# Kernel tuning notes

Hardware: AMD Instinct MI355X
Metric: run time of the kernel (lower is better)

## Reference

```python
import jax, jax.numpy as jnp
from jax import lax
import numpy as np

B, H, W = 8, 512, 512
HW = H * W  # sentinel label for non-mask pixels


def _label_components(mask):
    """4-connectivity connected-component labeling (min flat-index per component).
    mask: [H,W] bool. Returns [HW] int32 labels; non-mask pixels get label HW.
    Label propagation + pointer jumping -> O(log diameter) iterations."""
    idx = jnp.arange(HW, dtype=jnp.int32).reshape(H, W)
    lab0 = jnp.where(mask, idx, HW)

    def step(lab):
        p = jnp.pad(lab, 1, mode='constant', constant_values=HW)
        nb = jnp.minimum(jnp.minimum(p[:-2, 1:-1], p[2:, 1:-1]),
                         jnp.minimum(p[1:-1, :-2], p[1:-1, 2:]))
        new = jnp.where(mask, jnp.minimum(lab, nb), HW)
        flat = new.reshape(-1)
        flat_ext = jnp.concatenate([flat, jnp.array([HW], dtype=flat.dtype)])
        new = jnp.minimum(flat, flat_ext[flat]).reshape(H, W)  # pointer jump
        return jnp.where(mask, new, HW)

    def cond(state):
        return state[1]

    def body(state):
        lab, _ = state
        new = step(lab)
        return new, jnp.any(new != lab)

    lab, _ = lax.while_loop(cond, body, (lab0, jnp.array(True)))
    return lab.reshape(-1)


def _keep_large(mask):
    """Keep pixels belonging to components with area > max_area/2 (matches
    ndi.label + ndi.sum + thresholded relabel; ndi.sum scaling by 255/1 cancels)."""
    labels = _label_components(mask)  # [HW]
    counts = jax.ops.segment_sum(mask.reshape(-1).astype(jnp.float32), labels,
                                 num_segments=HW + 1)  # counts[HW]=0 (non-mask contributes 0)
    max_area = counts.max()
    keep = mask.reshape(-1) & (counts[labels] > 0.5 * max_area)
    return keep.reshape(mask.shape)


def _masked_ce(logits, target):
    """CrossEntropyLoss(ignore_index=255, reduction='mean'). logits [B,C,H,W], target [B,H,W]."""
    logp = jax.nn.log_softmax(logits, axis=1)
    valid = target != 255
    tc = jnp.where(valid, target, 0)
    nll = -jnp.take_along_axis(logp, tc[:, None], axis=1)[:, 0]  # [B,H,W]
    denom = jnp.maximum(jnp.sum(valid), 1).astype(logp.dtype)
    return jnp.sum(jnp.where(valid, nll, 0.0)) / denom


def setup_inputs() -> dict:
    key = jax.random.key(0)
    k1, k2 = jax.random.split(key)
    preds = jax.random.normal(k1, (3, B, 2, H, W), dtype=jnp.float32)
    cams = jax.random.uniform(k2, (B, 1, H, W), dtype=jnp.float32)
    return {"preds": preds, "cams": cams}


def reference(preds, cams):
    cam = cams[:, 0]                      # [B,H,W]
    bg_mask = cam >= 0.2                  # pixels left at 255 in bg_label (the labeled regions)
    fg_mask = cam > 0.6                   # pixels set to 1 in fg_label
    keep_bg = jax.vmap(_keep_large)(bg_mask)
    keep_fg = jax.vmap(_keep_large)(fg_mask)
    bg_t = jnp.where(keep_bg, 255, 0).astype(jnp.int32)   # large uncertain regions ignored
    fg_t = jnp.where(keep_fg, 1, 255).astype(jnp.int32)   # small/non-fg ignored
    loss = jnp.float32(0.0)
    for i in range(preds.shape[0]):       # weight (1**i / 1) == 1
        loss = loss + _masked_ce(preds[i], fg_t) + _masked_ce(preds[i], bg_t)
    return loss
```

## Files before the change

### kernel.cpp

```cpp
#include <hip/hip_runtime.h>
#include <hip/hip_bf16.h>
#include <math.h>

#define Bsz    8
#define Wdim   512
#define HWv    (512 * 512)
#define LOG2HW 18
#define NIMG   16
#define TILE   64
#define TPIX   (TILE * TILE)
#define CEBLK  6144
#define CNTBLK 2048


__device__ __forceinline__ int uf_find(int* L, int x) {
  int p = L[x];
  while (p != x) {
    int gp = L[p];
    if (gp != p) atomicMin(&L[x], gp);
    x = gp;
    p = L[x];
  }
  return x;
}

__device__ __forceinline__ int find_ro(const int* __restrict__ L, int x) {
  int p = L[x];
  while (p != x) { x = p; p = L[x]; }
  return x;
}

__device__ __forceinline__ void uf_union(int* L, int a, int b) {
  a = uf_find(L, a);
  b = uf_find(L, b);
  while (a != b) {
    if (a < b) { int t = a; a = b; b = t; }
    int old = atomicMin(&L[a], b);
    if (old == a) return;
    a = old;
  }
}


__global__ __launch_bounds__(1024) void k_local(const float* __restrict__ cams,
                                                int* __restrict__ labels,
                                                int* __restrict__ areas) {
  int img  = blockIdx.x >> 6;
  int tile = blockIdx.x & 63;
  int tY = tile >> 3, tX = tile & 7;
  int b = img & 7;
  bool fg = (img & 8) != 0;
  int gbase = img << LOG2HW;
  int oy = tY * TILE, ox = tX * TILE;
  int lane = threadIdx.x & 63;

  __shared__ int P[TPIX];
  __shared__ int A[TPIX];

  #pragma unroll
  for (int it = 0; it < 4; ++it) {
    int i  = it * 1024 + threadIdx.x;
    int ly = i >> 6;
    float c = cams[(b << LOG2HW) + ((oy + ly) << 9) + (ox + lane)];
    bool m = fg ? (c > 0.6f) : (c >= 0.2f);
    unsigned long long bm = __ballot(m);
    int par = -1;
    if (m) {
      unsigned long long below = (1ULL << lane) - 1ULL;
      unsigned long long z = (~bm) & below;
      int rs = z ? (64 - __clzll(z)) : 0;
      par = (ly << 6) + rs;
    }
    P[i] = par;
    A[i] = 0;
  }
  __syncthreads();

  #pragma unroll
  for (int it = 0; it < 4; ++it) {
    int i = it * 1024 + threadIdx.x;
    if (i >= TILE && P[i] >= 0 && P[i - TILE] >= 0) {
      bool skip = (lane > 0) && (P[i - 1] >= 0) && (P[i - TILE - 1] >= 0);
      if (!skip) uf_union(P, i, i - TILE);
    }
  }
  __syncthreads();

  #pragma unroll
  for (int it = 0; it < 4; ++it) {
    int i = it * 1024 + threadIdx.x;
    bool m = P[i] >= 0;
    unsigned long long bm = __ballot(m);
    int rs = 0;
    if (m) {
      unsigned long long below = (1ULL << lane) - 1ULL;
      unsigned long long z = (~bm) & below;
      rs = z ? (64 - __clzll(z)) : 0;
    }
    bool isStart = m && (rs == lane);
    int r = -1;
    if (isStart) r = find_ro(P, i);
    int root = __shfl(r, rs);
    if (m) P[i] = root;
    if (isStart) {
      unsigned long long t = (~bm) >> lane;
      int runlen = t ? (__ffsll((long long)t) - 1) : (64 - lane);
      atomicAdd(&A[root], runlen);
    }
  }
  __syncthreads();

  #pragma unroll
  for (int it = 0; it < 4; ++it) {
    int i  = it * 1024 + threadIdx.x;
    int ly = i >> 6;
    int g  = ((oy + ly) << 9) + (ox + lane);
    int p  = P[i];
    int lab = -1;
    if (p >= 0) lab = ((oy + (p >> 6)) << 9) + (ox + (p & 63));
    labels[gbase + g] = lab;
    areas[gbase + g]  = (p == i) ? A[i] : 0;
  }
}

__global__ void k_border(int* __restrict__ labels, int* __restrict__ maxa) {
  if (blockIdx.x == 0) {
    if (threadIdx.x < NIMG) maxa[threadIdx.x] = 0;
  }
  const int per_img = 14 * Wdim;
  int t = blockIdx.x * blockDim.x + threadIdx.x;
  if (t >= NIMG * per_img) return;
  int img = t / per_img;
  int r   = t - img * per_img;
  int k = r >> 9, j = r & (Wdim - 1);
  int* L = labels + (img << LOG2HW);
  if (k < 7) {
    int x = TILE * k + (TILE - 1);
    int p = (j << 9) + x, q = p + 1;
    if (L[p] >= 0 && L[q] >= 0) {
      bool skip = (j > 0) && (L[p - Wdim] >= 0) && (L[q - Wdim] >= 0);
      if (!skip) uf_union(L, p, q);
    }
  } else {
    int y = TILE * (k - 7) + (TILE - 1);
    int p = (y << 9) + j, q = p + Wdim;
    if (L[p] >= 0 && L[q] >= 0) {
      bool skip = (j > 0) && (L[p - 1] >= 0) && (L[q - 1] >= 0);
      if (!skip) uf_union(L, p, q);
    }
  }
}

__global__ void k_flatten(int* __restrict__ labels, int* __restrict__ areas) {
  int t = blockIdx.x * blockDim.x + threadIdx.x;
  int idx0 = t << 2;
  int4 ar = *(const int4*)&areas[idx0];
  if ((ar.x | ar.y | ar.z | ar.w) <= 0) return;
  int img  = idx0 >> LOG2HW;
  int base = img << LOG2HW;
  int* L = labels + base;
  int self0 = idx0 - base;
  int4 lab = *(const int4*)&labels[idx0];
  if (ar.x > 0) { int r = find_ro(L, lab.x); L[self0]     = r; if (r != self0)     atomicAdd(&areas[base + r], ar.x); }
  if (ar.y > 0) { int r = find_ro(L, lab.y); L[self0 + 1] = r; if (r != self0 + 1) atomicAdd(&areas[base + r], ar.y); }
  if (ar.z > 0) { int r = find_ro(L, lab.z); L[self0 + 2] = r; if (r != self0 + 2) atomicAdd(&areas[base + r], ar.z); }
  if (ar.w > 0) { int r = find_ro(L, lab.w); L[self0 + 3] = r; if (r != self0 + 3) atomicAdd(&areas[base + r], ar.w); }
}

__global__ void k_max(const int* __restrict__ areas, int* __restrict__ maxa) {
  int img = blockIdx.x >> 4;
  int seg = blockIdx.x & 15;
  const int4* a4 = (const int4*)(areas + (img << LOG2HW));
  int base = seg * (HWv / 4 / 16);
  int m = 0;
  #pragma unroll
  for (int k = 0; k < 16; ++k) {
    int4 v = a4[base + k * 256 + threadIdx.x];
    m = max(m, max(max(v.x, v.y), max(v.z, v.w)));
  }
  #pragma unroll
  for (int off = 32; off > 0; off >>= 1)
    m = max(m, __shfl_down(m, off));
  __shared__ int lm[4];
  int wave = threadIdx.x >> 6;
  if ((threadIdx.x & 63) == 0) lm[wave] = m;
  __syncthreads();
  if (threadIdx.x == 0) {
    int bm = max(max(lm[0], lm[1]), max(lm[2], lm[3]));
    if (bm > 0) atomicMax(&maxa[img], bm);
  }
}

__global__ __launch_bounds__(1024) void k_verdict(const int* __restrict__ labels,
                                                  const int* __restrict__ areas,
                                                  const int* __restrict__ maxa,
                                                  unsigned long long* __restrict__ bitsBG,
                                                  unsigned long long* __restrict__ bitsFG) {
  int img  = blockIdx.x >> 6;
  int tile = blockIdx.x & 63;
  int tY = tile >> 3, tX = tile & 7;
  int oy = tY * TILE, ox = tX * TILE;
  int base = img << LOG2HW;
  int mx = maxa[img];

  __shared__ int V[TPIX];

  int i  = threadIdx.x << 2;
  int ly = i >> 6, lx = i & 63;
  int g  = ((oy + ly) << 9) + (ox + lx);
  int4 lb = *(const int4*)&labels[base + g];
  int4 ar = *(const int4*)&areas[base + g];
  if (ar.x > 0) { V[i + 0] = (2 * areas[base + lb.x] > mx); lb.x = g + 0; }
  if (ar.y > 0) { V[i + 1] = (2 * areas[base + lb.y] > mx); lb.y = g + 1; }
  if (ar.z > 0) { V[i + 2] = (2 * areas[base + lb.z] > mx); lb.z = g + 2; }
  if (ar.w > 0) { V[i + 3] = (2 * areas[base + lb.w] > mx); lb.w = g + 3; }
  __syncthreads();

  int l[4] = {lb.x, lb.y, lb.z, lb.w};
  unsigned nib = 0;
  #pragma unroll
  for (int j = 0; j < 4; ++j) {
    if (l[j] >= 0) {
      int loc = (((l[j] >> 9) & 63) << 6) | (l[j] & 63);
      nib |= (V[loc] ? 1u : 0u) << j;
    }
  }

  int lane = threadIdx.x & 63;
  unsigned long long w = (unsigned long long)nib << ((lane & 15) << 2);
  w |= __shfl_xor(w, 1);
  w |= __shfl_xor(w, 2);
  w |= __shfl_xor(w, 4);
  w |= __shfl_xor(w, 8);
  if ((lane & 15) == 0) {
    int wordIdx = ((oy + ly) << 3) + tX;
    unsigned long long* dst = (img < 8) ? (bitsBG + ((img & 7) << 12))
                                        : (bitsFG + ((img & 7) << 12));
    dst[wordIdx] = w;
  }
}

__global__ __launch_bounds__(256) void k_ce(const float* __restrict__ preds,
                                            const unsigned long long* __restrict__ bitsBG,
                                            const unsigned long long* __restrict__ bitsFG,
                                            float* __restrict__ pf,
                                            float* __restrict__ pbg,
                                            int* __restrict__ pcf,
                                            int* __restrict__ pcb) {
  int tid = blockIdx.x * 256 + threadIdx.x;
  int g4  = tid & 65535;
  int pb  = tid >> 16;
  int b   = pb & 7;
  int p   = pb >> 3;

  int wi = (b << 12) + (g4 >> 4);
  int sh = (g4 & 15) << 2;
  unsigned nB = (unsigned)(bitsBG[wi] >> sh) & 15u;
  unsigned nF = (unsigned)(bitsFG[wi] >> sh) & 15u;

  const float* pbase = preds + ((size_t)((p * Bsz + b) * 2) << LOG2HW);
  int px = g4 << 2;
  float4 A0 = *(const float4*)&pbase[px];
  float4 A1 = *(const float4*)&pbase[HWv + px];

  float d[4] = {A0.x - A1.x, A0.y - A1.y, A0.z - A1.z, A0.w - A1.w};
  float sfg = 0.f, sbg = 0.f;
  #pragma unroll
  for (int j = 0; j < 4; ++j) {
    float sp = logf(1.f + expf(-fabsf(d[j])));
    bool vfj = (nF >> j) & 1u;
    bool vbj = !((nB >> j) & 1u);
    sfg += vfj ? (fmaxf(d[j], 0.f) + sp) : 0.f;
    sbg += vbj ? (fmaxf(-d[j], 0.f) + sp) : 0.f;
  }
  int cf = __popc(nF);
  int cb = 4 - __popc(nB);

  #pragma unroll
  for (int off = 32; off > 0; off >>= 1) {
    sfg += __shfl_down(sfg, off);
    sbg += __shfl_down(sbg, off);
    cf  += __shfl_down(cf, off);
    cb  += __shfl_down(cb, off);
  }
  __shared__ float lsf[4], lsb[4];
  __shared__ int   lcf[4], lcb[4];
  int wave = threadIdx.x >> 6;
  if ((threadIdx.x & 63) == 0) {
    lsf[wave] = sfg; lsb[wave] = sbg; lcf[wave] = cf; lcb[wave] = cb;
  }
  __syncthreads();
  if (threadIdx.x == 0) {
    pf[blockIdx.x]  = lsf[0] + lsf[1] + lsf[2] + lsf[3];
    pbg[blockIdx.x] = lsb[0] + lsb[1] + lsb[2] + lsb[3];
    if (p == 0) {
      pcf[blockIdx.x] = lcf[0] + lcf[1] + lcf[2] + lcf[3];
      pcb[blockIdx.x] = lcb[0] + lcb[1] + lcb[2] + lcb[3];
    }
  }
}

__global__ __launch_bounds__(1024) void k_final(const float* __restrict__ pf,
                                                const float* __restrict__ pbg,
                                                const int* __restrict__ pcf,
                                                const int* __restrict__ pcb,
                                                float* __restrict__ out) {
  int t = threadIdx.x;
  double sf = 0.0, sb = 0.0;
  int cf = 0, cb = 0;
  #pragma unroll
  for (int k = 0; k < CEBLK / 1024; ++k) {
    sf += (double)pf[k * 1024 + t];
    sb += (double)pbg[k * 1024 + t];
  }
  #pragma unroll
  for (int k = 0; k < CNTBLK / 1024; ++k) {
    cf += pcf[k * 1024 + t];
    cb += pcb[k * 1024 + t];
  }
  #pragma unroll
  for (int off = 32; off > 0; off >>= 1) {
    sf += __shfl_down(sf, off);
    sb += __shfl_down(sb, off);
    cf += __shfl_down(cf, off);
    cb += __shfl_down(cb, off);
  }
  __shared__ double dsf[16], dsb[16];
  __shared__ int    icf[16], icb[16];
  int wave = t >> 6;
  if ((t & 63) == 0) { dsf[wave] = sf; dsb[wave] = sb; icf[wave] = cf; icb[wave] = cb; }
  __syncthreads();
  if (t == 0) {
    double tf = 0.0, tb = 0.0; int af_ = 0, ab_ = 0;
    #pragma unroll
    for (int w = 0; w < 16; ++w) { tf += dsf[w]; tb += dsb[w]; af_ += icf[w]; ab_ += icb[w]; }
    double df = af_ > 0 ? (double)af_ : 1.0;
    double db = ab_ > 0 ? (double)ab_ : 1.0;
    out[0] = (float)(tf / df + tb / db);
  }
}

extern "C" void kernel_launch(void* const* d_in, const int* in_sizes, int n_in,
                              void* d_out, int out_size, void* d_ws, size_t ws_size,
                              hipStream_t stream) {
  (void)in_sizes; (void)n_in; (void)out_size; (void)ws_size;
  const float* preds = (const float*)d_in[0];
  const float* cams  = (const float*)d_in[1];
  float* out = (float*)d_out;

  int* labels = (int*)d_ws;
  int* areas  = labels + NIMG * HWv;
  int* maxa   = areas + NIMG * HWv;
  double* sums = (double*)(maxa + 16);
  int* counts  = (int*)(sums + 2);
  unsigned long long* bitsBG = (unsigned long long*)(counts + 2);
  unsigned long long* bitsFG = bitsBG + Bsz * (HWv / 64);
  float* pf  = (float*)(bitsFG + Bsz * (HWv / 64));
  float* pbg = pf + CEBLK;
  int*   pcf = (int*)(pbg + CEBLK);
  int*   pcb = pcf + CNTBLK;

  const int threads = 256;

  k_local  <<<NIMG * 64, 1024, 0, stream>>>(cams, labels, areas);
  k_border <<<(NIMG * 14 * Wdim + threads - 1) / threads, threads, 0, stream>>>(labels, maxa);
  k_flatten<<<NIMG * HWv / (threads * 4), threads, 0, stream>>>(labels, areas);
  k_max    <<<NIMG * 16, threads, 0, stream>>>(areas, maxa);
  k_verdict<<<NIMG * 64, 1024, 0, stream>>>(labels, areas, maxa, bitsBG, bitsFG);
  k_ce     <<<CEBLK, 256, 0, stream>>>(preds, bitsBG, bitsFG, pf, pbg, pcf, pcb);
  k_final  <<<1, 1024, 0, stream>>>(pf, pbg, pcf, pcb, out);
}
```

Before: 155.0 us.

## Replace dense area arrays with per-tile compact root lists for CCL

Each tile's local connected-component roots are recorded in a compact per-tile list, along with their packed areas. The dense areas array write, the full-image flatten scan and the full-image max scan are removed. Flattening, area accumulation, max tracking and verdicts now iterate only over root entries, and pixel bits are produced by a separate dense pass that gathers a per-root byte verdict. Block size of the local kernel drops to 512 threads. This adds extra launches, a root-list workspace and a shared atomic counter, and the verdict gather becomes scattered global byte reads.

```diff
diff --git a/kernel.cpp b/kernel.cpp
--- a/kernel.cpp
+++ b/kernel.cpp
@@ -9,8 +9,11 @@
 #define NIMG   16
 #define TILE   64
 #define TPIX   (TILE * TILE)
+#define NTILE  (NIMG * 64)
+#define LCAP   2048
 #define CEBLK  6144
 #define CNTBLK 2048
+#define NBORD  448
 
 
 __device__ __forceinline__ int uf_find(int* L, int x) {
@@ -42,9 +45,10 @@
 }
 
 
-__global__ __launch_bounds__(1024) void k_local(const float* __restrict__ cams,
-                                                int* __restrict__ labels,
-                                                int* __restrict__ areas) {
+__global__ __launch_bounds__(512) void k_local(const float* __restrict__ cams,
+                                               int* __restrict__ labels,
+                                               int* __restrict__ rootlist,
+                                               int* __restrict__ rootcnt) {
   int img  = blockIdx.x >> 6;
   int tile = blockIdx.x & 63;
   int tY = tile >> 3, tX = tile & 7;
@@ -56,10 +60,12 @@
 
   __shared__ int P[TPIX];
   __shared__ int A[TPIX];
-
-  #pragma unroll
-  for (int it = 0; it < 4; ++it) {
-    int i  = it * 1024 + threadIdx.x;
+  __shared__ int lcount;
+  if (threadIdx.x == 0) lcount = 0;
+
+  #pragma unroll
+  for (int it = 0; it < 8; ++it) {
+    int i  = it * 512 + threadIdx.x;
     int ly = i >> 6;
     float c = cams[(b << LOG2HW) + ((oy + ly) << 9) + (ox + lane)];
     bool m = fg ? (c > 0.6f) : (c >= 0.2f);
@@ -77,8 +83,8 @@
   __syncthreads();
 
   #pragma unroll
-  for (int it = 0; it < 4; ++it) {
-    int i = it * 1024 + threadIdx.x;
+  for (int it = 0; it < 8; ++it) {
+    int i = it * 512 + threadIdx.x;
     if (i >= TILE && P[i] >= 0 && P[i - TILE] >= 0) {
       bool skip = (lane > 0) && (P[i - 1] >= 0) && (P[i - TILE - 1] >= 0);
       if (!skip) uf_union(P, i, i - TILE);
@@ -87,8 +93,8 @@
   __syncthreads();
 
   #pragma unroll
-  for (int it = 0; it < 4; ++it) {
-    int i = it * 1024 + threadIdx.x;
+  for (int it = 0; it < 8; ++it) {
+    int i = it * 512 + threadIdx.x;
     bool m = P[i] >= 0;
     unsigned long long bm = __ballot(m);
     int rs = 0;
@@ -110,20 +116,44 @@
   }
   __syncthreads();
 
-  #pragma unroll
-  for (int it = 0; it < 4; ++it) {
-    int i  = it * 1024 + threadIdx.x;
+  int lbase = blockIdx.x << 11;
+  #pragma unroll
+  for (int it = 0; it < 8; ++it) {
+    int i  = it * 512 + threadIdx.x;
     int ly = i >> 6;
     int g  = ((oy + ly) << 9) + (ox + lane);
     int p  = P[i];
     int lab = -1;
     if (p >= 0) lab = ((oy + (p >> 6)) << 9) + (ox + (p & 63));
     labels[gbase + g] = lab;
-    areas[gbase + g]  = (p == i) ? A[i] : 0;
-  }
-}
-
-__global__ void k_border(int* __restrict__ labels, int* __restrict__ maxa) {
+    if (p == i) {
+      int pos = atomicAdd(&lcount, 1);
+      rootlist[lbase + pos] = (A[i] << 12) | i;
+    }
+  }
+  __syncthreads();
+  if (threadIdx.x == 0) rootcnt[blockIdx.x] = lcount;
+}
+
+__global__ void k_border(int* __restrict__ labels, int* __restrict__ maxa,
+                         const int* __restrict__ rootlist,
+                         const int* __restrict__ rootcnt,
+                         int* __restrict__ areasF) {
+  if (blockIdx.x >= NBORD) {
+    int tileg = blockIdx.x - NBORD;
+    int img  = tileg >> 6;
+    int tile = tileg & 63;
+    int tY = tile >> 3, tX = tile & 7;
+    int oy = tY * TILE, ox = tX * TILE;
+    int cnt = rootcnt[tileg];
+    int lbase = tileg << 11;
+    for (int e = threadIdx.x; e < cnt; e += 256) {
+      int i = rootlist[lbase + e] & 4095;
+      int g = ((oy + (i >> 6)) << 9) + (ox + (i & 63));
+      areasF[(img << LOG2HW) + g] = 0;
+    }
+    return;
+  }
   if (blockIdx.x == 0) {
     if (threadIdx.x < NIMG) maxa[threadIdx.x] = 0;
   }
@@ -151,39 +181,37 @@
   }
 }
 
-__global__ void k_flatten(int* __restrict__ labels, int* __restrict__ areas) {
-  int t = blockIdx.x * blockDim.x + threadIdx.x;
-  int idx0 = t << 2;
-  int4 ar = *(const int4*)&areas[idx0];
-  if ((ar.x | ar.y | ar.z | ar.w) <= 0) return;
-  int img  = idx0 >> LOG2HW;
-  int base = img << LOG2HW;
-  int* L = labels + base;
-  int self0 = idx0 - base;
-  int4 lab = *(const int4*)&labels[idx0];
-  if (ar.x > 0) { int r = find_ro(L, lab.x); L[self0]     = r; if (r != self0)     atomicAdd(&areas[base + r], ar.x); }
-  if (ar.y > 0) { int r = find_ro(L, lab.y); L[self0 + 1] = r; if (r != self0 + 1) atomicAdd(&areas[base + r], ar.y); }
-  if (ar.z > 0) { int r = find_ro(L, lab.z); L[self0 + 2] = r; if (r != self0 + 2) atomicAdd(&areas[base + r], ar.z); }
-  if (ar.w > 0) { int r = find_ro(L, lab.w); L[self0 + 3] = r; if (r != self0 + 3) atomicAdd(&areas[base + r], ar.w); }
-}
-
-__global__ void k_max(const int* __restrict__ areas, int* __restrict__ maxa) {
-  int img = blockIdx.x >> 4;
-  int seg = blockIdx.x & 15;
-  const int4* a4 = (const int4*)(areas + (img << LOG2HW));
-  int base = seg * (HWv / 4 / 16);
-  int m = 0;
-  #pragma unroll
-  for (int k = 0; k < 16; ++k) {
-    int4 v = a4[base + k * 256 + threadIdx.x];
-    m = max(m, max(max(v.x, v.y), max(v.z, v.w)));
+__global__ __launch_bounds__(256) void k_flat2(int* __restrict__ labels,
+                                               const int* __restrict__ rootlist,
+                                               const int* __restrict__ rootcnt,
+                                               int* __restrict__ areasF,
+                                               int* __restrict__ maxa) {
+  int tileg = blockIdx.x;
+  int img  = tileg >> 6;
+  int tile = tileg & 63;
+  int tY = tile >> 3, tX = tile & 7;
+  int oy = tY * TILE, ox = tX * TILE;
+  int cnt = rootcnt[tileg];
+  int lbase = tileg << 11;
+  int* L = labels + (img << LOG2HW);
+  int* AF = areasF + (img << LOG2HW);
+  int mymax = 0;
+  for (int e = threadIdx.x; e < cnt; e += 256) {
+    int ent  = rootlist[lbase + e];
+    int i    = ent & 4095;
+    int area = ent >> 12;
+    int g = ((oy + (i >> 6)) << 9) + (ox + (i & 63));
+    int fr = find_ro(L, g);
+    L[g] = fr;
+    int prev = atomicAdd(&AF[fr], area);
+    mymax = max(mymax, prev + area);
   }
   #pragma unroll
   for (int off = 32; off > 0; off >>= 1)
-    m = max(m, __shfl_down(m, off));
+    mymax = max(mymax, __shfl_down(mymax, off));
   __shared__ int lm[4];
   int wave = threadIdx.x >> 6;
-  if ((threadIdx.x & 63) == 0) lm[wave] = m;
+  if ((threadIdx.x & 63) == 0) lm[wave] = mymax;
   __syncthreads();
   if (threadIdx.x == 0) {
     int bm = max(max(lm[0], lm[1]), max(lm[2], lm[3]));
@@ -191,40 +219,44 @@
   }
 }
 
-__global__ __launch_bounds__(1024) void k_verdict(const int* __restrict__ labels,
-                                                  const int* __restrict__ areas,
-                                                  const int* __restrict__ maxa,
-                                                  unsigned long long* __restrict__ bitsBG,
-                                                  unsigned long long* __restrict__ bitsFG) {
-  int img  = blockIdx.x >> 6;
-  int tile = blockIdx.x & 63;
+__global__ __launch_bounds__(256) void k_verd_root(const int* __restrict__ labels,
+                                                   const int* __restrict__ rootlist,
+                                                   const int* __restrict__ rootcnt,
+                                                   const int* __restrict__ areasF,
+                                                   const int* __restrict__ maxa,
+                                                   unsigned char* __restrict__ verdictB) {
+  int tileg = blockIdx.x;
+  int img  = tileg >> 6;
+  int tile = tileg & 63;
   int tY = tile >> 3, tX = tile & 7;
   int oy = tY * TILE, ox = tX * TILE;
-  int base = img << LOG2HW;
+  int cnt = rootcnt[tileg];
+  int lbase = tileg << 11;
   int mx = maxa[img];
-
-  __shared__ int V[TPIX];
-
-  int i  = threadIdx.x << 2;
-  int ly = i >> 6, lx = i & 63;
-  int g  = ((oy + ly) << 9) + (ox + lx);
-  int4 lb = *(const int4*)&labels[base + g];
-  int4 ar = *(const int4*)&areas[base + g];
-  if (ar.x > 0) { V[i + 0] = (2 * areas[base + lb.x] > mx); lb.x = g + 0; }
-  if (ar.y > 0) { V[i + 1] = (2 * areas[base + lb.y] > mx); lb.y = g + 1; }
-  if (ar.z > 0) { V[i + 2] = (2 * areas[base + lb.z] > mx); lb.z = g + 2; }
-  if (ar.w > 0) { V[i + 3] = (2 * areas[base + lb.w] > mx); lb.w = g + 3; }
-  __syncthreads();
-
-  int l[4] = {lb.x, lb.y, lb.z, lb.w};
+  const int* L  = labels + (img << LOG2HW);
+  const int* AF = areasF + (img << LOG2HW);
+  for (int e = threadIdx.x; e < cnt; e += 256) {
+    int i = rootlist[lbase + e] & 4095;
+    int g = ((oy + (i >> 6)) << 9) + (ox + (i & 63));
+    int tot = AF[L[g]];
+    verdictB[(img << LOG2HW) + g] = (2 * tot > mx) ? 1 : 0;
+  }
+}
+
+__global__ __launch_bounds__(256) void k_vbits(const int* __restrict__ labels,
+                                               const unsigned char* __restrict__ verdictB,
+                                               unsigned long long* __restrict__ bitsBG,
+                                               unsigned long long* __restrict__ bitsFG) {
+  int tid = blockIdx.x * 256 + threadIdx.x;
+  int img = tid >> 16;
+  int g4  = tid & 65535;
+  int4 lb = *(const int4*)&labels[(img << LOG2HW) + (g4 << 2)];
+  const unsigned char* V = verdictB + (img << LOG2HW);
   unsigned nib = 0;
-  #pragma unroll
-  for (int j = 0; j < 4; ++j) {
-    if (l[j] >= 0) {
-      int loc = (((l[j] >> 9) & 63) << 6) | (l[j] & 63);
-      nib |= (V[loc] ? 1u : 0u) << j;
-    }
-  }
+  if (lb.x >= 0) nib |= (unsigned)V[lb.x];
+  if (lb.y >= 0) nib |= (unsigned)V[lb.y] << 1;
+  if (lb.z >= 0) nib |= (unsigned)V[lb.z] << 2;
+  if (lb.w >= 0) nib |= (unsigned)V[lb.w] << 3;
 
   int lane = threadIdx.x & 63;
   unsigned long long w = (unsigned long long)nib << ((lane & 15) << 2);
@@ -233,7 +265,7 @@
   w |= __shfl_xor(w, 4);
   w |= __shfl_xor(w, 8);
   if ((lane & 15) == 0) {
-    int wordIdx = ((oy + ly) << 3) + tX;
+    int wordIdx = g4 >> 4;
     unsigned long long* dst = (img < 8) ? (bitsBG + ((img & 7) << 12))
                                         : (bitsFG + ((img & 7) << 12));
     dst[wordIdx] = w;
@@ -349,8 +381,8 @@
   float* out = (float*)d_out;
 
   int* labels = (int*)d_ws;
-  int* areas  = labels + NIMG * HWv;
-  int* maxa   = areas + NIMG * HWv;
+  int* areasF = labels + NIMG * HWv;
+  int* maxa   = areasF + NIMG * HWv;
   double* sums = (double*)(maxa + 16);
   int* counts  = (int*)(sums + 2);
   unsigned long long* bitsBG = (unsigned long long*)(counts + 2);
@@ -359,14 +391,17 @@
   float* pbg = pf + CEBLK;
   int*   pcf = (int*)(pbg + CEBLK);
   int*   pcb = pcf + CNTBLK;
+  int*   rootlist = pcb + CNTBLK;
+  int*   rootcnt  = rootlist + NTILE * LCAP;
+  unsigned char* verdictB = (unsigned char*)(rootcnt + NTILE);
 
   const int threads = 256;
 
-  k_local  <<<NIMG * 64, 1024, 0, stream>>>(cams, labels, areas);
-  k_border <<<(NIMG * 14 * Wdim + threads - 1) / threads, threads, 0, stream>>>(labels, maxa);
-  k_flatten<<<NIMG * HWv / (threads * 4), threads, 0, stream>>>(labels, areas);
-  k_max    <<<NIMG * 16, threads, 0, stream>>>(areas, maxa);
-  k_verdict<<<NIMG * 64, 1024, 0, stream>>>(labels, areas, maxa, bitsBG, bitsFG);
-  k_ce     <<<CEBLK, 256, 0, stream>>>(preds, bitsBG, bitsFG, pf, pbg, pcf, pcb);
-  k_final  <<<1, 1024, 0, stream>>>(pf, pbg, pcf, pcb, out);
-}
+  k_local    <<<NTILE, 512, 0, stream>>>(cams, labels, rootlist, rootcnt);
+  k_border   <<<NBORD + NTILE, threads, 0, stream>>>(labels, maxa, rootlist, rootcnt, areasF);
+  k_flat2    <<<NTILE, threads, 0, stream>>>(labels, rootlist, rootcnt, areasF, maxa);
+  k_verd_root<<<NTILE, threads, 0, stream>>>(labels, rootlist, rootcnt, areasF, maxa, verdictB);
+  k_vbits    <<<NIMG * HWv / 4 / threads, threads, 0, stream>>>(labels, verdictB, bitsBG, bitsFG);
+  k_ce       <<<CEBLK, threads, 0, stream>>>(preds, bitsBG, bitsFG, pf, pbg, pcf, pcb);
+  k_final    <<<1, 1024, 0, stream>>>(pf, pbg, pcf, pcb, out);
+}
```

New measurement: 157.1 us. Within noise of the previous version (+1.4%).

## Fuse final reduction into CE kernel via last-block pattern; write labels early

Applied to the files above, without the earlier changes.

The separate single-block final-reduction kernel is removed. The last CE block to finish now does the reduction, detected through an atomic completion counter that k_border resets, which saves one kernel launch. In k_local, global labels are now written directly from the root found in the run-compression pass instead of being stored back to shared memory and re-read in the final loop. The cost is an atomic and a threadfence per CE block, plus a serial tail in which one 256-thread block reduces all the partials.

```diff
diff --git a/kernel.cpp b/kernel.cpp
--- a/kernel.cpp
+++ b/kernel.cpp
@@ -89,6 +89,7 @@
   #pragma unroll
   for (int it = 0; it < 4; ++it) {
     int i = it * 1024 + threadIdx.x;
+    int ly = i >> 6;
     bool m = P[i] >= 0;
     unsigned long long bm = __ballot(m);
     int rs = 0;
@@ -101,7 +102,10 @@
     int r = -1;
     if (isStart) r = find_ro(P, i);
     int root = __shfl(r, rs);
-    if (m) P[i] = root;
+    int g = ((oy + ly) << 9) + (ox + lane);
+    int lab = -1;
+    if (m) lab = ((oy + (root >> 6)) << 9) + (ox + (root & 63));
+    labels[gbase + g] = lab;
     if (isStart) {
       unsigned long long t = (~bm) >> lane;
       int runlen = t ? (__ffsll((long long)t) - 1) : (64 - lane);
@@ -115,17 +119,15 @@
     int i  = it * 1024 + threadIdx.x;
     int ly = i >> 6;
     int g  = ((oy + ly) << 9) + (ox + lane);
-    int p  = P[i];
-    int lab = -1;
-    if (p >= 0) lab = ((oy + (p >> 6)) << 9) + (ox + (p & 63));
-    labels[gbase + g] = lab;
-    areas[gbase + g]  = (p == i) ? A[i] : 0;
-  }
-}
-
-__global__ void k_border(int* __restrict__ labels, int* __restrict__ maxa) {
+    areas[gbase + g] = (P[i] == i) ? A[i] : 0;
+  }
+}
+
+__global__ void k_border(int* __restrict__ labels, int* __restrict__ maxa,
+                         int* __restrict__ cedone) {
   if (blockIdx.x == 0) {
     if (threadIdx.x < NIMG) maxa[threadIdx.x] = 0;
+    if (threadIdx.x == 0) cedone[0] = 0;
   }
   const int per_img = 14 * Wdim;
   int t = blockIdx.x * blockDim.x + threadIdx.x;
@@ -246,7 +248,9 @@
                                             float* __restrict__ pf,
                                             float* __restrict__ pbg,
                                             int* __restrict__ pcf,
-                                            int* __restrict__ pcb) {
+                                            int* __restrict__ pcb,
+                                            int* __restrict__ cedone,
+                                            float* __restrict__ out) {
   int tid = blockIdx.x * 256 + threadIdx.x;
   int g4  = tid & 65535;
   int pb  = tid >> 16;
@@ -285,6 +289,7 @@
   }
   __shared__ float lsf[4], lsb[4];
   __shared__ int   lcf[4], lcb[4];
+  __shared__ int   amLast;
   int wave = threadIdx.x >> 6;
   if ((threadIdx.x & 63) == 0) {
     lsf[wave] = sfg; lsb[wave] = sbg; lcf[wave] = cf; lcb[wave] = cb;
@@ -297,46 +302,47 @@
       pcf[blockIdx.x] = lcf[0] + lcf[1] + lcf[2] + lcf[3];
       pcb[blockIdx.x] = lcb[0] + lcb[1] + lcb[2] + lcb[3];
     }
-  }
-}
-
-__global__ __launch_bounds__(1024) void k_final(const float* __restrict__ pf,
-                                                const float* __restrict__ pbg,
-                                                const int* __restrict__ pcf,
-                                                const int* __restrict__ pcb,
-                                                float* __restrict__ out) {
-  int t = threadIdx.x;
-  double sf = 0.0, sb = 0.0;
-  int cf = 0, cb = 0;
-  #pragma unroll
-  for (int k = 0; k < CEBLK / 1024; ++k) {
-    sf += (double)pf[k * 1024 + t];
-    sb += (double)pbg[k * 1024 + t];
-  }
-  #pragma unroll
-  for (int k = 0; k < CNTBLK / 1024; ++k) {
-    cf += pcf[k * 1024 + t];
-    cb += pcb[k * 1024 + t];
-  }
-  #pragma unroll
-  for (int off = 32; off > 0; off >>= 1) {
-    sf += __shfl_down(sf, off);
-    sb += __shfl_down(sb, off);
-    cf += __shfl_down(cf, off);
-    cb += __shfl_down(cb, off);
-  }
-  __shared__ double dsf[16], dsb[16];
-  __shared__ int    icf[16], icb[16];
-  int wave = t >> 6;
-  if ((t & 63) == 0) { dsf[wave] = sf; dsb[wave] = sb; icf[wave] = cf; icb[wave] = cb; }
-  __syncthreads();
-  if (t == 0) {
-    double tf = 0.0, tb = 0.0; int af_ = 0, ab_ = 0;
+    __threadfence();
+    int v = atomicAdd(cedone, 1);
+    amLast = (v == CEBLK - 1);
+  }
+  __syncthreads();
+
+  if (amLast) {
+    __threadfence();
+    int t = threadIdx.x;
+    double sf = 0.0, sb = 0.0;
+    int acf = 0, acb = 0;
     #pragma unroll
-    for (int w = 0; w < 16; ++w) { tf += dsf[w]; tb += dsb[w]; af_ += icf[w]; ab_ += icb[w]; }
-    double df = af_ > 0 ? (double)af_ : 1.0;
-    double db = ab_ > 0 ? (double)ab_ : 1.0;
-    out[0] = (float)(tf / df + tb / db);
+    for (int k = 0; k < CEBLK / 256; ++k) {
+      sf += (double)pf[k * 256 + t];
+      sb += (double)pbg[k * 256 + t];
+    }
+    #pragma unroll
+    for (int k = 0; k < CNTBLK / 256; ++k) {
+      acf += pcf[k * 256 + t];
+      acb += pcb[k * 256 + t];
+    }
+    #pragma unroll
+    for (int off = 32; off > 0; off >>= 1) {
+      sf  += __shfl_down(sf, off);
+      sb  += __shfl_down(sb, off);
+      acf += __shfl_down(acf, off);
+      acb += __shfl_down(acb, off);
+    }
+    __shared__ double dsf[4], dsb[4];
+    __shared__ int    icf[4], icb[4];
+    if ((t & 63) == 0) { dsf[wave] = sf; dsb[wave] = sb; icf[wave] = acf; icb[wave] = acb; }
+    __syncthreads();
+    if (t == 0) {
+      double tf = dsf[0] + dsf[1] + dsf[2] + dsf[3];
+      double tb = dsb[0] + dsb[1] + dsb[2] + dsb[3];
+      int af_ = icf[0] + icf[1] + icf[2] + icf[3];
+      int ab_ = icb[0] + icb[1] + icb[2] + icb[3];
+      double df = af_ > 0 ? (double)af_ : 1.0;
+      double db = ab_ > 0 ? (double)ab_ : 1.0;
+      out[0] = (float)(tf / df + tb / db);
+    }
   }
 }
 
@@ -359,14 +365,14 @@
   float* pbg = pf + CEBLK;
   int*   pcf = (int*)(pbg + CEBLK);
   int*   pcb = pcf + CNTBLK;
+  int*   cedone = pcb + CNTBLK;
 
   const int threads = 256;
 
   k_local  <<<NIMG * 64, 1024, 0, stream>>>(cams, labels, areas);
-  k_border <<<(NIMG * 14 * Wdim + threads - 1) / threads, threads, 0, stream>>>(labels, maxa);
+  k_border <<<(NIMG * 14 * Wdim + threads - 1) / threads, threads, 0, stream>>>(labels, maxa, cedone);
   k_flatten<<<NIMG * HWv / (threads * 4), threads, 0, stream>>>(labels, areas);
   k_max    <<<NIMG * 16, threads, 0, stream>>>(areas, maxa);
   k_verdict<<<NIMG * 64, 1024, 0, stream>>>(labels, areas, maxa, bitsBG, bitsFG);
-  k_ce     <<<CEBLK, 256, 0, stream>>>(preds, bitsBG, bitsFG, pf, pbg, pcf, pcb);
-  k_final  <<<1, 1024, 0, stream>>>(pf, pbg, pcf, pcb, out);
-}
+  k_ce     <<<CEBLK, threads, 0, stream>>>(preds, bitsBG, bitsFG, pf, pbg, pcf, pcb, cedone, out);
+}
```

New measurement: 303.1 us. 1.96x slower.
